# Performance work log

Measured on AMD Instinct MI355X. Metric: run time of the kernel, lower is better.

Reference implementation:

```python
import jax, jax.numpy as jnp
import numpy as np
import math

EMBED_DIM = 1024
NUM_HEADS = 16
HEAD_DIM = EMBED_DIM // NUM_HEADS
BATCH = 2
SEQ = 2048


def setup_inputs() -> dict:
    key = jax.random.key(0)
    ks = jax.random.split(key, 9)
    s = 1.0 / math.sqrt(EMBED_DIM)
    return {
        "x": jax.random.normal(ks[0], (BATCH, SEQ, EMBED_DIM), jnp.float32),
        "Wq": jax.random.normal(ks[1], (EMBED_DIM, EMBED_DIM), jnp.float32) * s,
        "bq": jnp.zeros((EMBED_DIM,), jnp.float32),
        "Wk": jax.random.normal(ks[2], (EMBED_DIM, EMBED_DIM), jnp.float32) * s,
        "bk": jnp.zeros((EMBED_DIM,), jnp.float32),
        "Wv": jax.random.normal(ks[3], (EMBED_DIM, EMBED_DIM), jnp.float32) * s,
        "bv": jnp.zeros((EMBED_DIM,), jnp.float32),
        "Wo": jax.random.normal(ks[4], (EMBED_DIM, EMBED_DIM), jnp.float32) * s,
        "bo": jnp.zeros((EMBED_DIM,), jnp.float32),
    }


def _rope_tables(seq_len, dim, dtype):
    inv_freq = 1.0 / (10000.0 ** (jnp.arange(0, dim, 2, dtype=jnp.float32) / dim))
    t = jnp.arange(seq_len, dtype=jnp.float32)
    freqs = jnp.einsum("i,j->ij", t, inv_freq)          # [S, D/2]
    emb = jnp.concatenate([freqs, freqs], axis=-1)       # [S, D]
    return jnp.cos(emb).astype(dtype), jnp.sin(emb).astype(dtype)


def _rotate_half(x):
    x1, x2 = jnp.split(x, 2, axis=-1)
    return jnp.concatenate([-x2, x1], axis=-1)


def _apply_rope(x, cos, sin):
    # x: [B, S, H, D]; cos/sin: [S, D] -> broadcast over batch & heads
    cos = cos[None, :, None, :]
    sin = sin[None, :, None, :]
    return x * cos + _rotate_half(x) * sin


def reference(x, Wq, bq, Wk, bk, Wv, bv, Wo, bo):
    B, S, E = x.shape
    H, D = NUM_HEADS, HEAD_DIM
    q = (x @ Wq + bq).reshape(B, S, H, D)
    k = (x @ Wk + bk).reshape(B, S, H, D)
    v = (x @ Wv + bv).reshape(B, S, H, D)
    cos, sin = _rope_tables(S, D, x.dtype)
    q = _apply_rope(q, cos, sin)
    k = _apply_rope(k, cos, sin)
    scale = 1.0 / math.sqrt(D)
    # scores: [B, H, S, S]
    scores = jnp.einsum("bqhd,bkhd->bhqk", q, k) * scale
    attn = jax.nn.softmax(scores, axis=-1)
    ctx = jnp.einsum("bhqk,bkhd->bqhd", attn, v).reshape(B, S, E)
    return ctx @ Wo + bo
```

## Files before the change

kernel.cpp:

```cpp
#include <hip/hip_runtime.h>
#include <math.h>

#define B_ 2
#define S_ 2048
#define E_ 1024
#define H_ 16
#define D_ 64
#define M_ (B_*S_)

typedef _Float16 f16x8 __attribute__((ext_vector_type(8)));
typedef float    f32x4 __attribute__((ext_vector_type(4)));

__device__ __forceinline__ ushort f2h(float f) {
    _Float16 h = (_Float16)f;
    return __builtin_bit_cast(ushort, h);
}

__device__ __forceinline__ void gload_lds16(const ushort* g, ushort* l) {
    __builtin_amdgcn_global_load_lds(
        (const __attribute__((address_space(1))) unsigned int*)g,
        (__attribute__((address_space(3))) unsigned int*)l, 16, 0, 0);
}

__global__ void rope_table_kernel(float* __restrict__ ct, float* __restrict__ st)
{
    int i = blockIdx.x * blockDim.x + threadIdx.x;
    if (i >= S_ * 32) return;
    int j = i & 31, pos = i >> 5;
    float invf = (float)pow(10000.0, -(double)j / 32.0);
    float ang  = (float)pos * invf;
    ct[i] = (float)cos((double)ang);
    st[i] = (float)sin((double)ang);
}

__global__ void cast_x_kernel(const float* __restrict__ x, ushort* __restrict__ xf)
{
    int i = (blockIdx.x * blockDim.x + threadIdx.x) * 4;
    float4 v = *(const float4*)&x[i];
    *(ushort4*)&xf[i] = make_ushort4(f2h(v.x), f2h(v.y), f2h(v.z), f2h(v.w));
}

__global__ void wtrans_kernel(const float* __restrict__ W0, const float* __restrict__ W1,
                              const float* __restrict__ W2, const float* __restrict__ W3,
                              ushort* __restrict__ WT)
{
    __shared__ float tile[32][33];
    const float* W = (blockIdx.z == 0) ? W0 : (blockIdx.z == 1) ? W1
                   : (blockIdx.z == 2) ? W2 : W3;
    const size_t zoff = (size_t)blockIdx.z * E_ * E_;
    const int tx = threadIdx.x & 31, ty = threadIdx.x >> 5;
    const int k0 = blockIdx.x * 32, nb = blockIdx.y * 32;
    #pragma unroll
    for (int i = 0; i < 4; i++) {
        int r = i * 8 + ty;
        tile[r][tx] = W[(size_t)(k0 + r) * E_ + nb + tx];
    }
    __syncthreads();
    #pragma unroll
    for (int i = 0; i < 4; i++) {
        int r = i * 8 + ty;
        WT[zoff + (size_t)(nb + r) * E_ + k0 + tx] = f2h(tile[tx][r]);
    }
}

#define GBM 128
#define GBN 128
#define GBK 32

__global__ __launch_bounds__(256, 3)
void gemm_f16(const ushort* __restrict__ A, const ushort* __restrict__ WTp,
              const float* __restrict__ b0, const float* __restrict__ b1,
              const float* __restrict__ b2,
              const float* __restrict__ ct, const float* __restrict__ st,
              ushort* __restrict__ outQ, ushort* __restrict__ outK,
              ushort* __restrict__ outV, float* __restrict__ outF,
              int force_mode)
{
    __shared__ __align__(16) ushort lA[GBM * GBK];
    __shared__ __align__(16) ushort lB[GBN * GBK];

    const int tid  = threadIdx.x;
    const int wv   = tid >> 6, lane = tid & 63;
    const int c    = lane & 15, qd = lane >> 4;
    const int rh   = wv >> 1, chn = wv & 1;

    const int mode = (force_mode >= 0) ? force_mode : (int)blockIdx.z;
    const size_t zoff = (force_mode >= 0) ? 0 : (size_t)blockIdx.z * (E_ * E_);
    const ushort* Bt = WTp + zoff;

    const int m0 = blockIdx.y * GBM, n0 = blockIdx.x * GBN;

    const ushort* gsrc = (wv < 2) ? A : Bt;
    ushort* ldst = (wv < 2) ? lA : lB;
    const int rowbase = ((wv < 2) ? m0 : n0) + (wv & 1) * 64;
    const int lofs = (wv & 1) * 64 * GBK;
    const int srow = lane >> 2;
    const int soct = (lane & 3) * 8;

    f32x4 acc[4][4] = {};

    for (int k0i = 0; k0i < E_; k0i += GBK) {
        #pragma unroll
        for (int cc = 0; cc < 4; cc++) {
            const ushort* g = gsrc + (size_t)(rowbase + cc * 16 + srow) * E_ + k0i + soct;
            gload_lds16(g, ldst + lofs + cc * 512);
        }
        __syncthreads();

        f16x8 af[4], bf[4];
        #pragma unroll
        for (int mt = 0; mt < 4; mt++)
            af[mt] = *(const f16x8*)&lA[(rh * 64 + mt * 16 + c) * GBK + qd * 8];
        #pragma unroll
        for (int nt = 0; nt < 4; nt++)
            bf[nt] = *(const f16x8*)&lB[(chn * 64 + nt * 16 + c) * GBK + qd * 8];
        #pragma unroll
        for (int mt = 0; mt < 4; mt++)
            #pragma unroll
            for (int nt = 0; nt < 4; nt++)
                acc[mt][nt] = __builtin_amdgcn_mfma_f32_16x16x32_f16(af[mt], bf[nt], acc[mt][nt], 0, 0, 0);
        __syncthreads();
    }

    const float* bias = (mode == 0) ? b0 : (mode == 1) ? b1 : (mode == 2) ? b2 : b0;
    const int colbase = n0 + chn * 64;

    if (mode == 3) {
        #pragma unroll
        for (int mt = 0; mt < 4; mt++)
            #pragma unroll
            for (int r = 0; r < 4; r++) {
                const int row = m0 + rh * 64 + mt * 16 + qd * 4 + r;
                #pragma unroll
                for (int nt = 0; nt < 4; nt++) {
                    const int col = colbase + nt * 16 + c;
                    outF[(size_t)row * E_ + col] = acc[mt][nt][r] + bias[col];
                }
            }
    } else if (mode == 2) {
        const int hd = colbase >> 6;
        #pragma unroll
        for (int mt = 0; mt < 4; mt++)
            #pragma unroll
            for (int r = 0; r < 4; r++) {
                const int row = m0 + rh * 64 + mt * 16 + qd * 4 + r;
                const int bb = row >> 11, sl = row & (S_ - 1);
                const size_t base = ((size_t)(bb * H_ + hd) * (S_ / 8) + (sl >> 3)) * 512 + (sl & 7);
                #pragma unroll
                for (int nt = 0; nt < 4; nt++) {
                    const int d = nt * 16 + c;
                    outV[base + (size_t)d * 8] = f2h(acc[mt][nt][r] + bias[colbase + d]);
                }
            }
    } else {
        ushort* O = (mode == 0) ? outQ : outK;
        const float sc = (mode == 0) ? 0.125f : 1.0f;
        #pragma unroll
        for (int mt = 0; mt < 4; mt++)
            #pragma unroll
            for (int r = 0; r < 4; r++) {
                const int row = m0 + rh * 64 + mt * 16 + qd * 4 + r;
                const int pos = row & (S_ - 1);
                #pragma unroll
                for (int p = 0; p < 2; p++) {
                    const int j32 = p * 16 + c;
                    const float cth = ct[pos * 32 + j32], sth = st[pos * 32 + j32];
                    const float v1 = acc[mt][p][r]     + bias[colbase + p * 16 + c];
                    const float v2 = acc[mt][p + 2][r] + bias[colbase + (p + 2) * 16 + c];
                    O[(size_t)row * E_ + colbase + p * 16 + c]       = f2h((v1 * cth - v2 * sth) * sc);
                    O[(size_t)row * E_ + colbase + (p + 2) * 16 + c] = f2h((v2 * cth + v1 * sth) * sc);
                }
            }
    }
}

#define PST 80

__global__ __launch_bounds__(256, 4)
void attn_mfma(const ushort* __restrict__ Qf, const ushort* __restrict__ Kf,
               const ushort* __restrict__ Vf, ushort* __restrict__ ctxf)
{
    __shared__ ushort Kls[64 * PST];
    __shared__ ushort Vls[8 * 520];
    __shared__ ushort Pls[4 * 16 * PST];

    const int tid  = threadIdx.x;
    const int wv   = tid >> 6;
    const int lane = tid & 63;
    const int c    = lane & 15;
    const int qd   = lane >> 4;

    const int ntq = S_ / 64;
    const int bh  = blockIdx.x / ntq;
    const int qt  = blockIdx.x % ntq;
    const int b   = bh >> 4, h = bh & 15;
    const int q0  = qt * 64;

    const size_t qbase = ((size_t)b * S_ + q0) * E_ + h * 64;
    const size_t kbase = (size_t)b * S_ * E_ + h * 64;
    const size_t vbase = (size_t)bh * S_ * 64;

    const int r0 = tid >> 3,        dc0 = (tid & 7) * 8;
    const int r1 = (tid + 256) >> 3, dc1 = dc0;
    const int e0 = tid * 8,         e1 = (tid + 256) * 8;

    *(uint4*)&Kls[r0 * PST + dc0] = *(const uint4*)&Qf[qbase + (size_t)r0 * E_ + dc0];
    *(uint4*)&Kls[r1 * PST + dc1] = *(const uint4*)&Qf[qbase + (size_t)r1 * E_ + dc1];
    __syncthreads();
    f16x8 qfrag[2];
    {
        const int qrow = wv * 16 + c;
        #pragma unroll
        for (int kc = 0; kc < 2; kc++)
            qfrag[kc] = *(const f16x8*)&Kls[qrow * PST + kc * 32 + qd * 8];
    }
    __syncthreads();

    f32x4 acc[4] = {};
    float lsum[4] = {0.0f, 0.0f, 0.0f, 0.0f};

    uint4 kpre0 = *(const uint4*)&Kf[kbase + (size_t)r0 * E_ + dc0];
    uint4 kpre1 = *(const uint4*)&Kf[kbase + (size_t)r1 * E_ + dc1];
    uint4 vpre0 = *(const uint4*)&Vf[vbase + e0];
    uint4 vpre1 = *(const uint4*)&Vf[vbase + e1];

    for (int k0 = 0; k0 < S_; k0 += 64) {
        *(uint4*)&Kls[r0 * PST + dc0] = kpre0;
        *(uint4*)&Kls[r1 * PST + dc1] = kpre1;
        *(uint4*)&Vls[(e0 >> 9) * 520 + (e0 & 511)] = vpre0;
        *(uint4*)&Vls[(e1 >> 9) * 520 + (e1 & 511)] = vpre1;
        __syncthreads();

        if (k0 + 64 < S_) {
            kpre0 = *(const uint4*)&Kf[kbase + (size_t)(k0 + 64 + r0) * E_ + dc0];
            kpre1 = *(const uint4*)&Kf[kbase + (size_t)(k0 + 64 + r1) * E_ + dc1];
            vpre0 = *(const uint4*)&Vf[vbase + (size_t)(k0 + 64) * 64 + e0];
            vpre1 = *(const uint4*)&Vf[vbase + (size_t)(k0 + 64) * 64 + e1];
        }

        f32x4 sv[4];
        #pragma unroll
        for (int t = 0; t < 4; t++) {
            f32x4 s = {};
            #pragma unroll
            for (int kc = 0; kc < 2; kc++) {
                f16x8 kf = *(const f16x8*)&Kls[(t * 16 + c) * PST + kc * 32 + qd * 8];
                s = __builtin_amdgcn_mfma_f32_16x16x32_f16(qfrag[kc], kf, s, 0, 0, 0);
            }
            sv[t] = s;
        }
        #pragma unroll
        for (int t = 0; t < 4; t++)
            #pragma unroll
            for (int r = 0; r < 4; r++) {
                const float p = __expf(sv[t][r]);
                sv[t][r] = p;
                lsum[r] += p;
            }

        ushort* Pw = &Pls[wv * 16 * PST];
        #pragma unroll
        for (int t = 0; t < 4; t++)
            #pragma unroll
            for (int r = 0; r < 4; r++)
                Pw[(qd * 4 + r) * PST + t * 16 + c] = f2h(sv[t][r]);

        f16x8 pfrag[2];
        #pragma unroll
        for (int kc = 0; kc < 2; kc++)
            pfrag[kc] = *(const f16x8*)&Pw[c * PST + kc * 32 + qd * 8];

        #pragma unroll
        for (int dt = 0; dt < 4; dt++) {
            #pragma unroll
            for (int kc = 0; kc < 2; kc++) {
                const int kg = kc * 4 + qd;
                f16x8 vfr = *(const f16x8*)&Vls[kg * 520 + (dt * 16 + c) * 8];
                acc[dt] = __builtin_amdgcn_mfma_f32_16x16x32_f16(pfrag[kc], vfr, acc[dt], 0, 0, 0);
            }
        }
        __syncthreads();
    }

    #pragma unroll
    for (int r = 0; r < 4; r++) {
        float l = lsum[r];
        l += __shfl_xor(l, 1);
        l += __shfl_xor(l, 2);
        l += __shfl_xor(l, 4);
        l += __shfl_xor(l, 8);
        const float inv = 1.0f / l;
        const int row = q0 + wv * 16 + qd * 4 + r;
        #pragma unroll
        for (int dt = 0; dt < 4; dt++) {
            const size_t idx = ((size_t)b * S_ + row) * E_ + h * 64 + dt * 16 + c;
            ctxf[idx] = f2h(acc[dt][r] * inv);
        }
    }
}

extern "C" void kernel_launch(void* const* d_in, const int* in_sizes, int n_in,
                              void* d_out, int out_size, void* d_ws, size_t ws_size,
                              hipStream_t stream)
{
    const float* x  = (const float*)d_in[0];
    const float* Wq = (const float*)d_in[1];
    const float* bq = (const float*)d_in[2];
    const float* Wk = (const float*)d_in[3];
    const float* bk = (const float*)d_in[4];
    const float* Wv = (const float*)d_in[5];
    const float* bv = (const float*)d_in[6];
    const float* Wo = (const float*)d_in[7];
    const float* bo = (const float*)d_in[8];
    float* out = (float*)d_out;

    ushort* Qb = (ushort*)d_ws;
    ushort* Kb = Qb + (size_t)M_ * E_;
    ushort* Vf = Kb + (size_t)M_ * E_;
    ushort* xf = Vf + (size_t)M_ * E_;
    ushort* WT = xf + (size_t)M_ * E_;
    float*  ct = (float*)(WT + (size_t)4 * E_ * E_);
    float*  st = ct + S_ * 32;
    ushort* ctxf = Qb;

    hipLaunchKernelGGL(rope_table_kernel, dim3(256), dim3(256), 0, stream, ct, st);
    hipLaunchKernelGGL(cast_x_kernel, dim3((M_ * E_ / 4) / 256), dim3(256), 0, stream, x, xf);
    hipLaunchKernelGGL(wtrans_kernel, dim3(32, 32, 4), dim3(256), 0, stream,
                       Wq, Wk, Wv, Wo, WT);

    hipLaunchKernelGGL(gemm_f16, dim3(E_ / GBN, M_ / GBM, 3), dim3(256), 0, stream,
                       xf, WT, bq, bk, bv, ct, st,
                       Qb, Kb, Vf, (float*)nullptr, -1);

    hipLaunchKernelGGL(attn_mfma, dim3(B_ * H_ * (S_ / 64)), dim3(256), 0, stream,
                       Qb, Kb, Vf, ctxf);

    hipLaunchKernelGGL(gemm_f16, dim3(E_ / GBN, M_ / GBM, 1), dim3(256), 0, stream,
                       ctxf, WT + (size_t)3 * E_ * E_, bo, bo, bo, ct, st,
                       (ushort*)nullptr, (ushort*)nullptr, (ushort*)nullptr, out, 3);
}
```

Measured before the change: 215.1 us.

## Merge prep kernels and keep attention P in registers via transposed MFMA

Merges the rope-table, x-cast and weight-transpose kernels into a single launch that dispatches on block index, cutting two kernel launches. In attention, the score and PV MFMAs swap their operands so each lane holds one query row. The P tile is packed with cvt_pkrtz and redistributed with shuffles instead of going through LDS, which removes the Pls buffer and its stores. It also permits a higher occupancy bound and gives a simpler row-sum reduction and vectorized output stores. The risks are the added shuffle cost, round-toward-zero conversion of P, and register pressure under the tighter launch bound.

Measured after the change: 216.5 us. About the same (+0.7%).

```diff
diff --git a/kernel.cpp b/kernel.cpp
--- a/kernel.cpp
+++ b/kernel.cpp
@@ -9,6 +9,7 @@
 #define M_ (B_*S_)
 
 typedef _Float16 f16x8 __attribute__((ext_vector_type(8)));
+typedef __fp16   h16x2 __attribute__((ext_vector_type(2)));
 typedef float    f32x4 __attribute__((ext_vector_type(4)));
 
 __device__ __forceinline__ ushort f2h(float f) {
@@ -22,44 +23,44 @@
         (__attribute__((address_space(3))) unsigned int*)l, 16, 0, 0);
 }
 
-__global__ void rope_table_kernel(float* __restrict__ ct, float* __restrict__ st)
+__global__ void prep_kernel(const float* __restrict__ x,
+                            const float* __restrict__ W0, const float* __restrict__ W1,
+                            const float* __restrict__ W2, const float* __restrict__ W3,
+                            ushort* __restrict__ xf, ushort* __restrict__ WT,
+                            float* __restrict__ ct, float* __restrict__ st)
 {
-    int i = blockIdx.x * blockDim.x + threadIdx.x;
-    if (i >= S_ * 32) return;
-    int j = i & 31, pos = i >> 5;
-    float invf = (float)pow(10000.0, -(double)j / 32.0);
-    float ang  = (float)pos * invf;
-    ct[i] = (float)cos((double)ang);
-    st[i] = (float)sin((double)ang);
-}
-
-__global__ void cast_x_kernel(const float* __restrict__ x, ushort* __restrict__ xf)
-{
-    int i = (blockIdx.x * blockDim.x + threadIdx.x) * 4;
-    float4 v = *(const float4*)&x[i];
-    *(ushort4*)&xf[i] = make_ushort4(f2h(v.x), f2h(v.y), f2h(v.z), f2h(v.w));
-}
-
-__global__ void wtrans_kernel(const float* __restrict__ W0, const float* __restrict__ W1,
-                              const float* __restrict__ W2, const float* __restrict__ W3,
-                              ushort* __restrict__ WT)
-{
+    const int bid = blockIdx.x;
+    const int tid = threadIdx.x;
     __shared__ float tile[32][33];
-    const float* W = (blockIdx.z == 0) ? W0 : (blockIdx.z == 1) ? W1
-                   : (blockIdx.z == 2) ? W2 : W3;
-    const size_t zoff = (size_t)blockIdx.z * E_ * E_;
-    const int tx = threadIdx.x & 31, ty = threadIdx.x >> 5;
-    const int k0 = blockIdx.x * 32, nb = blockIdx.y * 32;
-    #pragma unroll
-    for (int i = 0; i < 4; i++) {
-        int r = i * 8 + ty;
-        tile[r][tx] = W[(size_t)(k0 + r) * E_ + nb + tx];
-    }
-    __syncthreads();
-    #pragma unroll
-    for (int i = 0; i < 4; i++) {
-        int r = i * 8 + ty;
-        WT[zoff + (size_t)(nb + r) * E_ + k0 + tx] = f2h(tile[tx][r]);
+
+    if (bid < 4096) {
+        const int z = bid >> 10, rem = bid & 1023;
+        const int k0 = (rem >> 5) * 32, nb = (rem & 31) * 32;
+        const float* W = (z == 0) ? W0 : (z == 1) ? W1 : (z == 2) ? W2 : W3;
+        const size_t zoff = (size_t)z * E_ * E_;
+        const int tx = tid & 31, ty = tid >> 5;
+        #pragma unroll
+        for (int i = 0; i < 4; i++) {
+            int r = i * 8 + ty;
+            tile[r][tx] = W[(size_t)(k0 + r) * E_ + nb + tx];
+        }
+        __syncthreads();
+        #pragma unroll
+        for (int i = 0; i < 4; i++) {
+            int r = i * 8 + ty;
+            WT[zoff + (size_t)(nb + r) * E_ + k0 + tx] = f2h(tile[tx][r]);
+        }
+    } else if (bid < 8192) {
+        const int i = (bid - 4096) * 1024 + tid * 4;
+        float4 v = *(const float4*)&x[i];
+        *(ushort4*)&xf[i] = make_ushort4(f2h(v.x), f2h(v.y), f2h(v.z), f2h(v.w));
+    } else {
+        const int i = (bid - 8192) * 256 + tid;
+        const int j = i & 31, pos = i >> 5;
+        float invf = (float)pow(10000.0, -(double)j / 32.0);
+        float ang  = (float)pos * invf;
+        ct[i] = (float)cos((double)ang);
+        st[i] = (float)sin((double)ang);
     }
 }
 
@@ -176,13 +177,12 @@
 
 #define PST 80
 
-__global__ __launch_bounds__(256, 4)
+__global__ __launch_bounds__(256, 6)
 void attn_mfma(const ushort* __restrict__ Qf, const ushort* __restrict__ Kf,
                const ushort* __restrict__ Vf, ushort* __restrict__ ctxf)
 {
     __shared__ ushort Kls[64 * PST];
     __shared__ ushort Vls[8 * 520];
-    __shared__ ushort Pls[4 * 16 * PST];
 
     const int tid  = threadIdx.x;
     const int wv   = tid >> 6;
@@ -200,9 +200,9 @@
     const size_t kbase = (size_t)b * S_ * E_ + h * 64;
     const size_t vbase = (size_t)bh * S_ * 64;
 
-    const int r0 = tid >> 3,        dc0 = (tid & 7) * 8;
+    const int r0 = tid >> 3,         dc0 = (tid & 7) * 8;
     const int r1 = (tid + 256) >> 3, dc1 = dc0;
-    const int e0 = tid * 8,         e1 = (tid + 256) * 8;
+    const int e0 = tid * 8,          e1 = (tid + 256) * 8;
 
     *(uint4*)&Kls[r0 * PST + dc0] = *(const uint4*)&Qf[qbase + (size_t)r0 * E_ + dc0];
     *(uint4*)&Kls[r1 * PST + dc1] = *(const uint4*)&Qf[qbase + (size_t)r1 * E_ + dc1];
@@ -217,12 +217,16 @@
     __syncthreads();
 
     f32x4 acc[4] = {};
-    float lsum[4] = {0.0f, 0.0f, 0.0f, 0.0f};
+    float lsum = 0.0f;
 
     uint4 kpre0 = *(const uint4*)&Kf[kbase + (size_t)r0 * E_ + dc0];
     uint4 kpre1 = *(const uint4*)&Kf[kbase + (size_t)r1 * E_ + dc1];
     uint4 vpre0 = *(const uint4*)&Vf[vbase + e0];
     uint4 vpre1 = *(const uint4*)&Vf[vbase + e1];
+
+    const int srcA = c + ((qd & 1) << 5);
+    const int srcB = srcA + 16;
+    const bool hi = qd >= 2;
 
     for (int k0 = 0; k0 < S_; k0 += 64) {
         *(uint4*)&Kls[r0 * PST + dc0] = kpre0;
@@ -245,7 +249,7 @@
             #pragma unroll
             for (int kc = 0; kc < 2; kc++) {
                 f16x8 kf = *(const f16x8*)&Kls[(t * 16 + c) * PST + kc * 32 + qd * 8];
-                s = __builtin_amdgcn_mfma_f32_16x16x32_f16(qfrag[kc], kf, s, 0, 0, 0);
+                s = __builtin_amdgcn_mfma_f32_16x16x32_f16(kf, qfrag[kc], s, 0, 0, 0);
             }
             sv[t] = s;
         }
@@ -255,20 +259,37 @@
             for (int r = 0; r < 4; r++) {
                 const float p = __expf(sv[t][r]);
                 sv[t][r] = p;
-                lsum[r] += p;
-            }
-
-        ushort* Pw = &Pls[wv * 16 * PST];
-        #pragma unroll
-        for (int t = 0; t < 4; t++)
-            #pragma unroll
-            for (int r = 0; r < 4; r++)
-                Pw[(qd * 4 + r) * PST + t * 16 + c] = f2h(sv[t][r]);
+                lsum += p;
+            }
+
+        unsigned int pk0[4], pk1[4];
+        #pragma unroll
+        for (int t = 0; t < 4; t++) {
+            h16x2 a   = __builtin_amdgcn_cvt_pkrtz(sv[t][0], sv[t][1]);
+            h16x2 bb2 = __builtin_amdgcn_cvt_pkrtz(sv[t][2], sv[t][3]);
+            pk0[t] = __builtin_bit_cast(unsigned int, a);
+            pk1[t] = __builtin_bit_cast(unsigned int, bb2);
+        }
 
         f16x8 pfrag[2];
         #pragma unroll
-        for (int kc = 0; kc < 2; kc++)
-            pfrag[kc] = *(const f16x8*)&Pw[c * PST + kc * 32 + qd * 8];
+        for (int kc = 0; kc < 2; kc++) {
+            const int t0 = kc * 2, t1 = kc * 2 + 1;
+            unsigned int s00 = (unsigned int)__shfl((int)pk0[t0], srcA);
+            unsigned int s01 = (unsigned int)__shfl((int)pk0[t1], srcA);
+            unsigned int s10 = (unsigned int)__shfl((int)pk1[t0], srcA);
+            unsigned int s11 = (unsigned int)__shfl((int)pk1[t1], srcA);
+            unsigned int s20 = (unsigned int)__shfl((int)pk0[t0], srcB);
+            unsigned int s21 = (unsigned int)__shfl((int)pk0[t1], srcB);
+            unsigned int s30 = (unsigned int)__shfl((int)pk1[t0], srcB);
+            unsigned int s31 = (unsigned int)__shfl((int)pk1[t1], srcB);
+            uint4 pd;
+            pd.x = hi ? s01 : s00;
+            pd.y = hi ? s11 : s10;
+            pd.z = hi ? s21 : s20;
+            pd.w = hi ? s31 : s30;
+            pfrag[kc] = __builtin_bit_cast(f16x8, pd);
+        }
 
         #pragma unroll
         for (int dt = 0; dt < 4; dt++) {
@@ -276,26 +297,23 @@
             for (int kc = 0; kc < 2; kc++) {
                 const int kg = kc * 4 + qd;
                 f16x8 vfr = *(const f16x8*)&Vls[kg * 520 + (dt * 16 + c) * 8];
-                acc[dt] = __builtin_amdgcn_mfma_f32_16x16x32_f16(pfrag[kc], vfr, acc[dt], 0, 0, 0);
-            }
-        }
-        __syncthreads();
-    }
-
+                acc[dt] = __builtin_amdgcn_mfma_f32_16x16x32_f16(vfr, pfrag[kc], acc[dt], 0, 0, 0);
+            }
+        }
+        __syncthreads();
+    }
+
+    float l = lsum;
+    l += __shfl_xor(l, 16);
+    l += __shfl_xor(l, 32);
+    const float inv = 1.0f / l;
+
+    const size_t orow = ((size_t)b * S_ + q0 + wv * 16 + c) * E_ + h * 64;
     #pragma unroll
-    for (int r = 0; r < 4; r++) {
-        float l = lsum[r];
-        l += __shfl_xor(l, 1);
-        l += __shfl_xor(l, 2);
-        l += __shfl_xor(l, 4);
-        l += __shfl_xor(l, 8);
-        const float inv = 1.0f / l;
-        const int row = q0 + wv * 16 + qd * 4 + r;
-        #pragma unroll
-        for (int dt = 0; dt < 4; dt++) {
-            const size_t idx = ((size_t)b * S_ + row) * E_ + h * 64 + dt * 16 + c;
-            ctxf[idx] = f2h(acc[dt][r] * inv);
-        }
+    for (int dt = 0; dt < 4; dt++) {
+        ushort4 o = make_ushort4(f2h(acc[dt][0] * inv), f2h(acc[dt][1] * inv),
+                                 f2h(acc[dt][2] * inv), f2h(acc[dt][3] * inv));
+        *(ushort4*)&ctxf[orow + dt * 16 + qd * 4] = o;
     }
 }
 
@@ -323,10 +341,8 @@
     float*  st = ct + S_ * 32;
     ushort* ctxf = Qb;
 
-    hipLaunchKernelGGL(rope_table_kernel, dim3(256), dim3(256), 0, stream, ct, st);
-    hipLaunchKernelGGL(cast_x_kernel, dim3((M_ * E_ / 4) / 256), dim3(256), 0, stream, x, xf);
-    hipLaunchKernelGGL(wtrans_kernel, dim3(32, 32, 4), dim3(256), 0, stream,
-                       Wq, Wk, Wv, Wo, WT);
+    hipLaunchKernelGGL(prep_kernel, dim3(8448), dim3(256), 0, stream,
+                       x, Wq, Wk, Wv, Wo, xf, WT, ct, st);
 
     hipLaunchKernelGGL(gemm_f16, dim3(E_ / GBN, M_ / GBM, 3), dim3(256), 0, stream,
                        xf, WT, bq, bk, bv, ct, st,
```
